# Kernel tuning notes

Hardware: AMD Instinct MI355X
Metric: run time of the kernel (lower is better)

Reference implementation:

```python
import jax, jax.numpy as jnp
import numpy as np

N_NODES = 100000
ORDER = 2


def _spmm(edge_src, edge_dst, edge_weight, x):
    # out[dst] += w * x[src]  ==  adj @ x  with adj in COO form
    msgs = edge_weight[:, None] * x[edge_src]          # [E, d]
    return jax.ops.segment_sum(msgs, edge_dst, num_segments=N_NODES)


def setup_inputs() -> dict:
    key = jax.random.key(0)
    k1, k2, k3, k4 = jax.random.split(key, 4)
    x = jax.random.normal(k1, (N_NODES, 32), dtype=jnp.float32)
    edge_src = jax.random.randint(k2, (1600000,), 0, N_NODES, dtype=jnp.int32)
    edge_dst = jax.random.randint(k3, (1600000,), 0, N_NODES, dtype=jnp.int32)
    edge_weight = jax.random.uniform(k4, (1600000,), dtype=jnp.float32)
    return {"x": x, "edge_src": edge_src, "edge_dst": edge_dst,
            "edge_weight": edge_weight}


def reference(x, edge_src, edge_dst, edge_weight):
    # SGConvolution.forward: x = spmm(adj, x) repeated `order` times
    for _ in range(ORDER):
        x = _spmm(edge_src, edge_dst, edge_weight, x)
    return x
```

## Files before the change

kernel.cpp:

```cpp
#include <hip/hip_runtime.h>

#define N_NODES 100000
#define NEDGE   1600000
#define D       32

#define BSHIFT   8
#define BNODES   256
#define NBUCKET  ((N_NODES + BNODES - 1) / BNODES)
#define NB_PAD   392
#define EPB      4096
#define EPT      (EPB / 256)
#define CBLK     ((NEDGE + EPB - 1) / EPB)
#define CAP      5120

__global__ __launch_bounds__(256) void bin_edges_kernel(
        const int* __restrict__ src, const int* __restrict__ dst,
        const float* __restrict__ w,
        int* __restrict__ bucket_cur, int2* __restrict__ binned) {
    __shared__ int2 sorted[EPB];
    __shared__ unsigned short bucketOf[EPB];
    __shared__ int cnt[NB_PAD];
    __shared__ int ndoff[NB_PAD];
    __shared__ int delta[NB_PAD];
    __shared__ int partial[256];

    const int tid = threadIdx.x;
    const int e0  = blockIdx.x * EPB;
    const int total = min(EPB, NEDGE - e0);

    for (int i = tid; i < NB_PAD; i += 256) cnt[i] = 0;
    __syncthreads();

    int myd[EPT];
    #pragma unroll
    for (int it = 0; it < EPT; ++it) {
        int e = e0 + it * 256 + tid;
        myd[it] = (e < NEDGE) ? dst[e] : -1;
        if (myd[it] >= 0) atomicAdd(&cnt[myd[it] >> BSHIFT], 1);
    }
    __syncthreads();

    {
        int b0 = tid * 2;
        int c0 = 0, c1 = 0, s = 0;
        if (b0 < NB_PAD) { c0 = cnt[b0]; c1 = cnt[b0 + 1]; s = c0 + c1; }
        partial[tid] = s;
        __syncthreads();
        int v = s;
        for (int o = 1; o < 256; o <<= 1) {
            int t2 = (tid >= o) ? partial[tid - o] : 0;
            __syncthreads();
            partial[tid] += t2;
            __syncthreads();
        }
        int run = partial[tid] - v;
        if (b0 < NB_PAD) {
            ndoff[b0] = run;
            if (c0 > 0) delta[b0] = b0 * CAP + atomicAdd(&bucket_cur[b0], c0) - run;
            cnt[b0] = 0;
            run += c0;
            ndoff[b0 + 1] = run;
            if (c1 > 0) delta[b0 + 1] = (b0 + 1) * CAP + atomicAdd(&bucket_cur[b0 + 1], c1) - run;
            cnt[b0 + 1] = 0;
            run += c1;
        }
    }
    __syncthreads();

    #pragma unroll
    for (int it = 0; it < EPT; ++it) {
        int d = myd[it];
        if (d >= 0) {
            int e = e0 + it * 256 + tid;
            int b = d >> BSHIFT;
            int r = atomicAdd(&cnt[b], 1);
            int loc = ndoff[b] + r;
            sorted[loc]   = make_int2(src[e] | ((d & (BNODES - 1)) << 17),
                                      __float_as_int(w[e]));
            bucketOf[loc] = (unsigned short)b;
        }
    }
    __syncthreads();

    for (int i = tid; i < total; i += 256) {
        int2 v = sorted[i];
        int  b = bucketOf[i];
        binned[delta[b] + i] = v;
    }
}

__global__ __launch_bounds__(256) void build_csr_kernel(
        const int* __restrict__ bucket_cur,
        int2* __restrict__ binned, int* __restrict__ offv, int* __restrict__ deg) {
    __shared__ int2 sorted[CAP];
    __shared__ int ndcnt[BNODES];
    __shared__ int ndoff[BNODES];

    int b = blockIdx.x;
    int tid = threadIdx.x;
    int start = b * CAP;
    int cnt_b = min(bucket_cur[b], CAP);

    ndcnt[tid] = 0;
    __syncthreads();

    for (int i = tid; i < cnt_b; i += 256)
        atomicAdd(&ndcnt[(binned[start + i].x >> 17) & (BNODES - 1)], 1);
    __syncthreads();

    int v = ndcnt[tid];
    ndoff[tid] = v;
    __syncthreads();
    for (int o = 1; o < BNODES; o <<= 1) {
        int t = (tid >= o) ? ndoff[tid - o] : 0;
        __syncthreads();
        ndoff[tid] += t;
        __syncthreads();
    }
    {
        int incl = ndoff[tid];
        __syncthreads();
        ndoff[tid] = incl - v;
        int node = b * BNODES + tid;
        if (node < N_NODES) {
            offv[node] = start + incl - v;
            deg[node]  = v;
        }
        ndcnt[tid] = 0;
    }
    __syncthreads();

    for (int i = tid; i < cnt_b; i += 256) {
        int2 p = binned[start + i];
        int dl = (p.x >> 17) & (BNODES - 1);
        int r = atomicAdd(&ndcnt[dl], 1);
        sorted[ndoff[dl] + r] = make_int2(p.x & 0x1FFFF, p.y);
    }
    __syncthreads();
    for (int i = tid; i < cnt_b; i += 256) binned[start + i] = sorted[i];
}

__global__ void spmm_gather_kernel(const int* __restrict__ off, const int* __restrict__ deg,
                                   const int2* __restrict__ csr_sw,
                                   const float* __restrict__ x, float* __restrict__ out) {
    int gid = blockIdx.x * blockDim.x + threadIdx.x;
    if (gid >= N_NODES * 8) return;
    int node = gid >> 3;
    int c    = gid & 7;
    int start = off[node];
    int len   = deg[node];
    float4 acc = {0.f, 0.f, 0.f, 0.f};
    int k = 0;
    for (; k + 4 <= len; k += 4) {
        int2 sw0 = csr_sw[start + k];
        int2 sw1 = csr_sw[start + k + 1];
        int2 sw2 = csr_sw[start + k + 2];
        int2 sw3 = csr_sw[start + k + 3];
        const float4 xv0 = *reinterpret_cast<const float4*>(&x[(long)sw0.x * D + c * 4]);
        const float4 xv1 = *reinterpret_cast<const float4*>(&x[(long)sw1.x * D + c * 4]);
        const float4 xv2 = *reinterpret_cast<const float4*>(&x[(long)sw2.x * D + c * 4]);
        const float4 xv3 = *reinterpret_cast<const float4*>(&x[(long)sw3.x * D + c * 4]);
        float w0 = __int_as_float(sw0.y), w1 = __int_as_float(sw1.y);
        float w2 = __int_as_float(sw2.y), w3 = __int_as_float(sw3.y);
        acc.x += w0 * xv0.x; acc.y += w0 * xv0.y; acc.z += w0 * xv0.z; acc.w += w0 * xv0.w;
        acc.x += w1 * xv1.x; acc.y += w1 * xv1.y; acc.z += w1 * xv1.z; acc.w += w1 * xv1.w;
        acc.x += w2 * xv2.x; acc.y += w2 * xv2.y; acc.z += w2 * xv2.z; acc.w += w2 * xv2.w;
        acc.x += w3 * xv3.x; acc.y += w3 * xv3.y; acc.z += w3 * xv3.z; acc.w += w3 * xv3.w;
    }
    for (; k < len; ++k) {
        int2 sw = csr_sw[start + k];
        const float4 xv = *reinterpret_cast<const float4*>(&x[(long)sw.x * D + c * 4]);
        float wt = __int_as_float(sw.y);
        acc.x += wt * xv.x; acc.y += wt * xv.y; acc.z += wt * xv.z; acc.w += wt * xv.w;
    }
    *reinterpret_cast<float4*>(&out[(long)node * D + c * 4]) = acc;
}

__global__ void spmm_scatter_kernel(const int* __restrict__ src, const int* __restrict__ dst,
                                    const float* __restrict__ w, const float* __restrict__ x,
                                    float* __restrict__ out) {
    long gid = (long)blockIdx.x * blockDim.x + threadIdx.x;
    if (gid >= (long)NEDGE * 8) return;
    int e = (int)(gid >> 3);
    int c = (int)(gid & 7);
    int s = src[e], d = dst[e];
    float wt = w[e];
    const float4 xv = *reinterpret_cast<const float4*>(&x[(long)s * D + c * 4]);
    float* o = &out[(long)d * D + c * 4];
    atomicAdd(o + 0, wt * xv.x);
    atomicAdd(o + 1, wt * xv.y);
    atomicAdd(o + 2, wt * xv.z);
    atomicAdd(o + 3, wt * xv.w);
}

extern "C" void kernel_launch(void* const* d_in, const int* in_sizes, int n_in,
                              void* d_out, int out_size, void* d_ws, size_t ws_size,
                              hipStream_t stream) {
    const float* x    = (const float*)d_in[0];
    const int*   esrc = (const int*)d_in[1];
    const int*   edst = (const int*)d_in[2];
    const float* ew   = (const float*)d_in[3];
    float* out = (float*)d_out;

    char* ws = (char*)d_ws;
    const size_t y_bytes   = (size_t)N_NODES * D * sizeof(float);
    const size_t n_ints    = (size_t)N_NODES * sizeof(int);
    const size_t b_ints    = (size_t)NB_PAD * sizeof(int);
    const size_t arena_sz  = (size_t)NBUCKET * CAP * sizeof(int2);

    size_t o = 0;
    float* y          = (float*)(ws + o); o += y_bytes;
    int2*  binned     = (int2*) (ws + o); o += arena_sz;
    int*   off        = (int*)  (ws + o); o += n_ints;
    int*   deg        = (int*)  (ws + o); o += n_ints;
    int*   bucket_cur = (int*)  (ws + o); o += b_ints;

    if (ws_size < o) {
        hipMemsetAsync(y, 0, y_bytes, stream);
        hipMemsetAsync(out, 0, y_bytes, stream);
        const long total = (long)NEDGE * 8;
        const int blocks = (int)((total + 255) / 256);
        spmm_scatter_kernel<<<blocks, 256, 0, stream>>>(esrc, edst, ew, x, y);
        spmm_scatter_kernel<<<blocks, 256, 0, stream>>>(esrc, edst, ew, y, out);
        return;
    }

    hipMemsetAsync(bucket_cur, 0, b_ints, stream);
    bin_edges_kernel<<<CBLK, 256, 0, stream>>>(esrc, edst, ew, bucket_cur, binned);
    build_csr_kernel<<<NBUCKET, 256, 0, stream>>>(bucket_cur, binned, off, deg);

    const int gblocks = (N_NODES * 8 + 255) / 256;
    spmm_gather_kernel<<<gblocks, 256, 0, stream>>>(off, deg, binned, x, y);
    spmm_gather_kernel<<<gblocks, 256, 0, stream>>>(off, deg, binned, y, out);
}
```

Before: 112.1 us.

## Replace global bucket atomics with per-block count tables and a prefix scan

The binning kernel now writes its locally sorted edges back contiguously into its own block region and records per-block bucket counts and offsets in tables, instead of scattering each edge to a global bucket arena through atomic-reserved slots. A new single-block scan computes bucket base offsets, and the CSR build kernel (now 512 threads) has one thread per source block read its bucket segment before node-level sorting, writing a compact CSR array. The aim is coalesced writes in binning and a compact CSR layout, at the cost of an extra kernel launch, strided table reads, and serial per-thread loops over short segments in the build step.

```diff
diff --git a/kernel.cpp b/kernel.cpp
--- a/kernel.cpp
+++ b/kernel.cpp
@@ -16,17 +16,17 @@
 __global__ __launch_bounds__(256) void bin_edges_kernel(
         const int* __restrict__ src, const int* __restrict__ dst,
         const float* __restrict__ w,
-        int* __restrict__ bucket_cur, int2* __restrict__ binned) {
+        int* __restrict__ total, int* __restrict__ tblc, int* __restrict__ tblo,
+        int2* __restrict__ binned) {
     __shared__ int2 sorted[EPB];
-    __shared__ unsigned short bucketOf[EPB];
     __shared__ int cnt[NB_PAD];
     __shared__ int ndoff[NB_PAD];
-    __shared__ int delta[NB_PAD];
     __shared__ int partial[256];
 
     const int tid = threadIdx.x;
-    const int e0  = blockIdx.x * EPB;
-    const int total = min(EPB, NEDGE - e0);
+    const int blk = blockIdx.x;
+    const int e0  = blk * EPB;
+    const int tot_e = min(EPB, NEDGE - e0);
 
     for (int i = tid; i < NB_PAD; i += 256) cnt[i] = 0;
     __syncthreads();
@@ -56,11 +56,15 @@
         int run = partial[tid] - v;
         if (b0 < NB_PAD) {
             ndoff[b0] = run;
-            if (c0 > 0) delta[b0] = b0 * CAP + atomicAdd(&bucket_cur[b0], c0) - run;
+            tblc[blk * NB_PAD + b0] = c0;
+            tblo[blk * NB_PAD + b0] = run;
+            if (c0 > 0) atomicAdd(&total[b0], c0);
             cnt[b0] = 0;
             run += c0;
             ndoff[b0 + 1] = run;
-            if (c1 > 0) delta[b0 + 1] = (b0 + 1) * CAP + atomicAdd(&bucket_cur[b0 + 1], c1) - run;
+            tblc[blk * NB_PAD + b0 + 1] = c1;
+            tblo[blk * NB_PAD + b0 + 1] = run;
+            if (c1 > 0) atomicAdd(&total[b0 + 1], c1);
             cnt[b0 + 1] = 0;
             run += c1;
         }
@@ -74,70 +78,89 @@
             int e = e0 + it * 256 + tid;
             int b = d >> BSHIFT;
             int r = atomicAdd(&cnt[b], 1);
-            int loc = ndoff[b] + r;
-            sorted[loc]   = make_int2(src[e] | ((d & (BNODES - 1)) << 17),
-                                      __float_as_int(w[e]));
-            bucketOf[loc] = (unsigned short)b;
-        }
-    }
-    __syncthreads();
-
-    for (int i = tid; i < total; i += 256) {
-        int2 v = sorted[i];
-        int  b = bucketOf[i];
-        binned[delta[b] + i] = v;
-    }
-}
-
-__global__ __launch_bounds__(256) void build_csr_kernel(
-        const int* __restrict__ bucket_cur,
-        int2* __restrict__ binned, int* __restrict__ offv, int* __restrict__ deg) {
+            sorted[ndoff[b] + r] = make_int2(src[e] | ((d & (BNODES - 1)) << 17),
+                                             __float_as_int(w[e]));
+        }
+    }
+    __syncthreads();
+
+    for (int i = tid; i < tot_e; i += 256)
+        binned[e0 + i] = sorted[i];
+}
+
+__global__ void bucket_scan_kernel(const int* __restrict__ total, int* __restrict__ base) {
+    __shared__ int s[512];
+    int tid = threadIdx.x;
+    int v = (tid < NB_PAD) ? total[tid] : 0;
+    s[tid] = v;
+    __syncthreads();
+    for (int o = 1; o < 512; o <<= 1) {
+        int t = (tid >= o) ? s[tid - o] : 0;
+        __syncthreads();
+        s[tid] += t;
+        __syncthreads();
+    }
+    if (tid < NB_PAD) base[tid] = s[tid] - v;
+}
+
+__global__ __launch_bounds__(512) void build_csr_kernel(
+        const int* __restrict__ total, const int* __restrict__ base,
+        const int* __restrict__ tblc, const int* __restrict__ tblo,
+        const int2* __restrict__ binned,
+        int2* __restrict__ csr, int* __restrict__ offv, int* __restrict__ deg) {
     __shared__ int2 sorted[CAP];
     __shared__ int ndcnt[BNODES];
     __shared__ int ndoff[BNODES];
 
-    int b = blockIdx.x;
-    int tid = threadIdx.x;
-    int start = b * CAP;
-    int cnt_b = min(bucket_cur[b], CAP);
-
-    ndcnt[tid] = 0;
-    __syncthreads();
-
-    for (int i = tid; i < cnt_b; i += 256)
-        atomicAdd(&ndcnt[(binned[start + i].x >> 17) & (BNODES - 1)], 1);
-    __syncthreads();
-
-    int v = ndcnt[tid];
-    ndoff[tid] = v;
+    const int b = blockIdx.x;
+    const int tid = threadIdx.x;
+
+    if (tid < BNODES) ndcnt[tid] = 0;
+    int rl = 0, ro = 0;
+    if (tid < CBLK) { rl = tblc[tid * NB_PAD + b]; ro = tblo[tid * NB_PAD + b]; }
+    const int s0 = tid * EPB + ro;
+    __syncthreads();
+
+    for (int i = 0; i < rl; ++i) {
+        int2 p = binned[s0 + i];
+        atomicAdd(&ndcnt[(p.x >> 17) & (BNODES - 1)], 1);
+    }
+    __syncthreads();
+
+    int v = (tid < BNODES) ? ndcnt[tid] : 0;
+    if (tid < BNODES) ndoff[tid] = v;
     __syncthreads();
     for (int o = 1; o < BNODES; o <<= 1) {
-        int t = (tid >= o) ? ndoff[tid - o] : 0;
-        __syncthreads();
-        ndoff[tid] += t;
-        __syncthreads();
-    }
-    {
+        int t = (tid < BNODES && tid >= o) ? ndoff[tid - o] : 0;
+        __syncthreads();
+        if (tid < BNODES) ndoff[tid] += t;
+        __syncthreads();
+    }
+    if (tid < BNODES) {
         int incl = ndoff[tid];
-        __syncthreads();
         ndoff[tid] = incl - v;
         int node = b * BNODES + tid;
         if (node < N_NODES) {
-            offv[node] = start + incl - v;
+            offv[node] = base[b] + incl - v;
             deg[node]  = v;
         }
         ndcnt[tid] = 0;
     }
     __syncthreads();
 
-    for (int i = tid; i < cnt_b; i += 256) {
-        int2 p = binned[start + i];
+    for (int i = 0; i < rl; ++i) {
+        int2 p = binned[s0 + i];
         int dl = (p.x >> 17) & (BNODES - 1);
         int r = atomicAdd(&ndcnt[dl], 1);
-        sorted[ndoff[dl] + r] = make_int2(p.x & 0x1FFFF, p.y);
-    }
-    __syncthreads();
-    for (int i = tid; i < cnt_b; i += 256) binned[start + i] = sorted[i];
+        int loc = ndoff[dl] + r;
+        if (loc < CAP) sorted[loc] = make_int2(p.x & 0x1FFFF, p.y);
+    }
+    __syncthreads();
+
+    const int totb = min(total[b], CAP);
+    const int bb = base[b];
+    for (int i = tid; i < totb; i += 512)
+        csr[bb + i] = sorted[i];
 }
 
 __global__ void spmm_gather_kernel(const int* __restrict__ off, const int* __restrict__ deg,
@@ -204,32 +227,40 @@
 
     char* ws = (char*)d_ws;
     const size_t y_bytes   = (size_t)N_NODES * D * sizeof(float);
+    const size_t bin_sz    = (size_t)CBLK * EPB * sizeof(int2);
+    const size_t csr_sz    = (size_t)NEDGE * sizeof(int2);
     const size_t n_ints    = (size_t)N_NODES * sizeof(int);
     const size_t b_ints    = (size_t)NB_PAD * sizeof(int);
-    const size_t arena_sz  = (size_t)NBUCKET * CAP * sizeof(int2);
+    const size_t t_ints    = (size_t)CBLK * NB_PAD * sizeof(int);
 
     size_t o = 0;
-    float* y          = (float*)(ws + o); o += y_bytes;
-    int2*  binned     = (int2*) (ws + o); o += arena_sz;
-    int*   off        = (int*)  (ws + o); o += n_ints;
-    int*   deg        = (int*)  (ws + o); o += n_ints;
-    int*   bucket_cur = (int*)  (ws + o); o += b_ints;
+    float* y      = (float*)(ws + o); o += y_bytes;
+    int2*  binned = (int2*) (ws + o); o += bin_sz;
+    int2*  csr    = (int2*) (ws + o); o += csr_sz;
+    int*   off    = (int*)  (ws + o); o += n_ints;
+    int*   deg    = (int*)  (ws + o); o += n_ints;
+    int*   total  = (int*)  (ws + o); o += b_ints;
+    int*   base   = (int*)  (ws + o); o += b_ints;
+    int*   tblc   = (int*)  (ws + o); o += t_ints;
+    int*   tblo   = (int*)  (ws + o); o += t_ints;
 
     if (ws_size < o) {
         hipMemsetAsync(y, 0, y_bytes, stream);
         hipMemsetAsync(out, 0, y_bytes, stream);
-        const long total = (long)NEDGE * 8;
-        const int blocks = (int)((total + 255) / 256);
+        const long tot = (long)NEDGE * 8;
+        const int blocks = (int)((tot + 255) / 256);
         spmm_scatter_kernel<<<blocks, 256, 0, stream>>>(esrc, edst, ew, x, y);
         spmm_scatter_kernel<<<blocks, 256, 0, stream>>>(esrc, edst, ew, y, out);
         return;
     }
 
-    hipMemsetAsync(bucket_cur, 0, b_ints, stream);
-    bin_edges_kernel<<<CBLK, 256, 0, stream>>>(esrc, edst, ew, bucket_cur, binned);
-    build_csr_kernel<<<NBUCKET, 256, 0, stream>>>(bucket_cur, binned, off, deg);
+    hipMemsetAsync(total, 0, b_ints, stream);
+    bin_edges_kernel<<<CBLK, 256, 0, stream>>>(esrc, edst, ew, total, tblc, tblo, binned);
+    bucket_scan_kernel<<<1, 512, 0, stream>>>(total, base);
+    build_csr_kernel<<<NBUCKET, 512, 0, stream>>>(total, base, tblc, tblo, binned,
+                                                  csr, off, deg);
 
     const int gblocks = (N_NODES * 8 + 255) / 256;
-    spmm_gather_kernel<<<gblocks, 256, 0, stream>>>(off, deg, binned, x, y);
-    spmm_gather_kernel<<<gblocks, 256, 0, stream>>>(off, deg, binned, y, out);
-}
+    spmm_gather_kernel<<<gblocks, 256, 0, stream>>>(off, deg, csr, x, y);
+    spmm_gather_kernel<<<gblocks, 256, 0, stream>>>(off, deg, csr, y, out);
+}
```

Result: slower. 130.8 us (+16.7%).
